# Performance work log

Measured on AMD Instinct MI355X. Metric: run time of the kernel, lower is better.

Reference implementation:

```python
import jax, jax.numpy as jnp
import numpy as np

N = 100000   # nodes
E = 1600000  # edges
G = 64       # graphs in batch
IN, H, F1, OUT = 3, 64, 256, 10
EPS = 1e-5


def setup_inputs() -> dict:
    key = jax.random.key(0)
    ks = jax.random.split(key, 16)
    d = {}
    d["x"] = jax.random.normal(ks[0], (N, IN), dtype=jnp.float32)
    d["membership"] = jnp.sort(jax.random.randint(ks[1], (N,), 0, G))
    d["edges"] = jax.random.randint(ks[2], (2, E), 0, N)
    def lin(k, fan_in, shape):
        return jax.random.uniform(k, shape, jnp.float32, -1.0, 1.0) / np.sqrt(fan_in)
    # GraphConv1: out = lin_rel(agg) + lin_root(x); lin_root has no bias in PyG
    d["W_rel1"] = lin(ks[3], IN, (IN, H)); d["b_rel1"] = jnp.zeros((H,), jnp.float32)
    d["W_root1"] = lin(ks[4], IN, (IN, H))
    d["W_rel2"] = lin(ks[5], H, (H, H)); d["b_rel2"] = jnp.zeros((H,), jnp.float32)
    d["W_root2"] = lin(ks[6], H, (H, H))
    d["g1"] = jnp.ones((H,), jnp.float32); d["b1"] = jnp.zeros((H,), jnp.float32)
    d["g2"] = jnp.ones((H,), jnp.float32); d["b2"] = jnp.zeros((H,), jnp.float32)
    d["W_fc1"] = lin(ks[7], H, (H, F1)); d["b_fc1"] = lin(ks[8], H, (F1,))
    d["g3"] = jnp.ones((F1,), jnp.float32); d["b3"] = jnp.zeros((F1,), jnp.float32)
    d["W_fc2"] = lin(ks[9], F1, (F1, OUT)); d["b_fc2"] = lin(ks[10], F1, (OUT,))
    return d


def _bn(h, g, b):
    # BatchNorm1d in training mode: biased batch variance
    m = h.mean(axis=0)
    v = h.var(axis=0)
    return (h - m) * jax.lax.rsqrt(v + EPS) * g + b


def reference(x, membership, edges, W_rel1, b_rel1, W_root1, W_rel2, b_rel2,
              W_root2, g1, b1, g2, b2, W_fc1, b_fc1, g3, b3, W_fc2, b_fc2):
    src, dst = edges[0], edges[1]

    def gconv(h, Wr, br, Wroot):
        # message = x_j (edge_weight=None); aggr='add' at target node
        agg = jax.ops.segment_sum(h[src], dst, num_segments=N)
        return agg @ Wr + br + h @ Wroot

    h = _bn(jax.nn.relu(gconv(x, W_rel1, b_rel1, W_root1)), g1, b1)
    h = _bn(jax.nn.relu(gconv(h, W_rel2, b_rel2, W_root2)), g2, b2)
    # global mean pool over graph membership
    cnt = jax.ops.segment_sum(jnp.ones((N,), h.dtype), membership, num_segments=G)
    pooled = jax.ops.segment_sum(h, membership, num_segments=G) / jnp.maximum(cnt, 1.0)[:, None]
    z = _bn(jax.nn.relu(pooled @ W_fc1 + b_fc1), g3, b3)
    return z @ W_fc2 + b_fc2
```

## Files before the change

kernel.cpp:

```cpp
#include <hip/hip_runtime.h>
#include <hip/hip_bf16.h>

#define EPSV 1e-5f
#define BKT 128
#define NB  782
#define LPK 4096

typedef __hip_bfloat16 bf16;
typedef __attribute__((ext_vector_type(8))) short short8v;
typedef __attribute__((ext_vector_type(4))) float f32x4v;

__device__ inline void atomAddG(float* p, float v) { unsafeAtomicAdd(p, v); }
__device__ inline unsigned short f2bf(float v) {
    bf16 h = __float2bfloat16(v);
    return *reinterpret_cast<unsigned short*>(&h);
}
__device__ inline float bfu(unsigned short u) {
    return __uint_as_float(((unsigned int)u) << 16);
}

__global__ __launch_bounds__(256) void bhist_kernel(
    const int* __restrict__ edges, int* __restrict__ gbcnt,
    const float* __restrict__ x, float* __restrict__ xp, int E, int N)
{
    __shared__ int lh[NB];
    const int t = threadIdx.x;
    for (int i = t; i < NB; i += 256) lh[i] = 0;
    {
        int n = blockIdx.x * 256 + t;
        if (n < N) {
            float4 v;
            v.x = x[n * 3 + 0]; v.y = x[n * 3 + 1]; v.z = x[n * 3 + 2]; v.w = 0.f;
            *(float4*)&xp[n * 4] = v;
        }
    }
    __syncthreads();
    const int base = blockIdx.x * 4096;
    #pragma unroll
    for (int i = 0; i < 16; ++i) {
        int e = base + i * 256 + t;
        if (e < E) atomicAdd(&lh[edges[E + e] >> 7], 1);
    }
    __syncthreads();
    for (int i = t; i < NB; i += 256) {
        int c = lh[i];
        if (c) atomicAdd(&gbcnt[i], c);
    }
}

__global__ __launch_bounds__(256) void bscan_kernel(
    const int* __restrict__ gbcnt, int* __restrict__ bbase,
    int* __restrict__ gcursor, int E)
{
    __shared__ int l[256];
    const int t = threadIdx.x;
    int b0 = t * 4;
    int v0 = (b0 + 0 < NB) ? gbcnt[b0 + 0] : 0;
    int v1 = (b0 + 1 < NB) ? gbcnt[b0 + 1] : 0;
    int v2 = (b0 + 2 < NB) ? gbcnt[b0 + 2] : 0;
    int v3 = (b0 + 3 < NB) ? gbcnt[b0 + 3] : 0;
    int tot = v0 + v1 + v2 + v3;
    l[t] = tot;
    __syncthreads();
    for (int o = 1; o < 256; o <<= 1) {
        int add = (t >= o) ? l[t - o] : 0;
        __syncthreads();
        l[t] += add;
        __syncthreads();
    }
    int off = l[t] - tot;
    if (b0 + 0 < NB) { bbase[b0 + 0] = off;                gcursor[b0 + 0] = off; }
    if (b0 + 1 < NB) { bbase[b0 + 1] = off + v0;           gcursor[b0 + 1] = off + v0; }
    if (b0 + 2 < NB) { bbase[b0 + 2] = off + v0 + v1;      gcursor[b0 + 2] = off + v0 + v1; }
    if (b0 + 3 < NB) { bbase[b0 + 3] = off + v0 + v1 + v2; gcursor[b0 + 3] = off + v0 + v1 + v2; }
    if (t == 0) bbase[NB] = E;
}

__global__ __launch_bounds__(256) void bfill_kernel(
    const int* __restrict__ edges, int* __restrict__ gcursor,
    int* __restrict__ pk,
    const int* __restrict__ membership, int* __restrict__ gstart, int E, int N)
{
    __shared__ int lh[NB];
    __shared__ int lbase[NB];
    const int t = threadIdx.x;
    for (int i = t; i < NB; i += 256) lh[i] = 0;
    {
        int n = blockIdx.x * 256 + t;
        if (n <= N) {
            int mp = (n == 0) ? -1 : membership[n - 1];
            int mc = (n == N) ? 64 : membership[n];
            for (int g = mp + 1; g <= mc; ++g) gstart[g] = n;
        }
    }
    __syncthreads();
    const int base = blockIdx.x * 4096;
    int dv[16];
    #pragma unroll
    for (int i = 0; i < 16; ++i) {
        int e = base + i * 256 + t;
        dv[i] = (e < E) ? edges[E + e] : -1;
        if (dv[i] >= 0) atomicAdd(&lh[dv[i] >> 7], 1);
    }
    __syncthreads();
    for (int i = t; i < NB; i += 256) {
        int c = lh[i];
        lbase[i] = c ? atomicAdd(&gcursor[i], c) : 0;
        lh[i] = 0;
    }
    __syncthreads();
    #pragma unroll
    for (int i = 0; i < 16; ++i) {
        int e = base + i * 256 + t;
        if (dv[i] >= 0) {
            int s = edges[e];
            int b = dv[i] >> 7;
            int pos = lbase[b] + atomicAdd(&lh[b], 1);
            pk[pos] = (s << 7) | (dv[i] & 127);
        }
    }
}

__global__ __launch_bounds__(256) void bsort_kernel(
    const int* __restrict__ pk, const int* __restrict__ bbase,
    const float* __restrict__ xp,
    int* __restrict__ rowstart, int* __restrict__ srcs,
    float* __restrict__ agg1, int N, int E)
{
    __shared__ int lcnt[BKT];
    __shared__ int lscan[BKT];
    __shared__ float accx[BKT * 4];
    __shared__ int lpk[LPK];
    const int t = threadIdx.x;
    const int b = blockIdx.x;
    const int e0 = bbase[b], e1 = bbase[b + 1];
    const int cnt = e1 - e0;
    if (t < BKT) lcnt[t] = 0;
    for (int i = t; i < BKT * 4; i += 256) accx[i] = 0.f;
    for (int i = t; i < cnt && i < LPK; i += 256) lpk[i] = pk[e0 + i];
    __syncthreads();
    for (int i = t; i < cnt; i += 256) {
        int v = (i < LPK) ? lpk[i] : pk[e0 + i];
        atomicAdd(&lcnt[v & 127], 1);
    }
    __syncthreads();
    if (t < BKT) lscan[t] = lcnt[t];
    __syncthreads();
    for (int o = 1; o < BKT; o <<= 1) {
        int add = (t < BKT && t >= o) ? lscan[t - o] : 0;
        __syncthreads();
        if (t < BKT) lscan[t] += add;
        __syncthreads();
    }
    const int n0 = b * BKT;
    if (t < BKT) {
        int excl = lscan[t] - lcnt[t];
        lscan[t] = excl;
        int n = n0 + t;
        if (n <= N) rowstart[n] = e0 + excl;
        lcnt[t] = 0;
    }
    __syncthreads();
    for (int i = t; i < cnt; i += 256) {
        int v = (i < LPK) ? lpk[i] : pk[e0 + i];
        int ld = v & 127;
        int s = v >> 7;
        int pos = atomicAdd(&lcnt[ld], 1);
        srcs[e0 + lscan[ld] + pos] = s;
        float4 xv = *(const float4*)&xp[s * 4];
        atomicAdd(&accx[ld * 4 + 0], xv.x);
        atomicAdd(&accx[ld * 4 + 1], xv.y);
        atomicAdd(&accx[ld * 4 + 2], xv.z);
    }
    __syncthreads();
    for (int i = t; i < BKT * 3; i += 256) {
        int nl = i / 3, c = i - nl * 3;
        int n = n0 + nl;
        if (n < N) agg1[n * 3 + c] = accx[nl * 4 + c];
    }
}

__global__ __launch_bounds__(256) void layer1_kernel(
    const float* __restrict__ x, const float* __restrict__ agg1,
    const float* __restrict__ W_rel1, const float* __restrict__ b_rel1,
    const float* __restrict__ W_root1,
    unsigned short* __restrict__ u1b, float* __restrict__ sums, float* __restrict__ sumsq,
    int N)
{
    const int t = threadIdx.x;
    const int f = t & 63, r4 = t >> 6;
    const float wr0 = W_rel1[f], wr1 = W_rel1[64 + f], wr2 = W_rel1[128 + f];
    const float wo0 = W_root1[f], wo1 = W_root1[64 + f], wo2 = W_root1[128 + f];
    const float bb = b_rel1[f];
    float ps = 0.f, pq = 0.f;
    const int base = blockIdx.x * 128;
    for (int i = r4; i < 128; i += 4) {
        int n = base + i;
        if (n >= N) break;
        float a0 = agg1[n * 3 + 0], a1 = agg1[n * 3 + 1], a2 = agg1[n * 3 + 2];
        float x0 = x[n * 3 + 0], x1 = x[n * 3 + 1], x2 = x[n * 3 + 2];
        float v = bb;
        v = fmaf(a0, wr0, v); v = fmaf(a1, wr1, v); v = fmaf(a2, wr2, v);
        v = fmaf(x0, wo0, v); v = fmaf(x1, wo1, v); v = fmaf(x2, wo2, v);
        v = fmaxf(v, 0.f);
        u1b[n * 64 + f] = f2bf(v);
        ps += v; pq += v * v;
    }
    __shared__ float lsum[4][64], lsq[4][64];
    lsum[r4][f] = ps; lsq[r4][f] = pq;
    __syncthreads();
    if (r4 == 0) {
        float s = lsum[0][f] + lsum[1][f] + lsum[2][f] + lsum[3][f];
        float q = lsq[0][f] + lsq[1][f] + lsq[2][f] + lsq[3][f];
        atomAddG(&sums[f], s);
        atomAddG(&sumsq[f], q);
    }
}

__global__ __launch_bounds__(256) void bnfold_kernel(
    const float* __restrict__ sums1, const float* __restrict__ sumsq1,
    const float* __restrict__ g1, const float* __restrict__ b1,
    const float* __restrict__ W_rel2, const float* __restrict__ W_root2,
    const float* __restrict__ b_rel2,
    unsigned short* __restrict__ wrelp, unsigned short* __restrict__ wrootp,
    float* __restrict__ crel, float* __restrict__ croot, float invn)
{
    __shared__ float lsc[64], lsh[64];
    __shared__ float r1[4][64], r2[4][64];
    const int t = threadIdx.x, f = t & 63, kg = t >> 6;
    if (t < 64) {
        float m = sums1[t] * invn;
        float v = sumsq1[t] * invn - m * m;
        float sc = g1[t] * rsqrtf(v + EPSV);
        lsc[t] = sc;
        lsh[t] = b1[t] - m * sc;
    }
    __syncthreads();
    float c1 = 0.f, c2 = 0.f;
    for (int k = kg * 16; k < kg * 16 + 16; ++k) {
        float sc = lsc[k], sh = lsh[k];
        float w1 = W_rel2[k * 64 + f], w2 = W_root2[k * 64 + f];
        wrelp[k * 64 + f] = f2bf(sc * w1);
        wrootp[k * 64 + f] = f2bf(sc * w2);
        c1 = fmaf(sh, w1, c1); c2 = fmaf(sh, w2, c2);
    }
    r1[kg][f] = c1; r2[kg][f] = c2;
    __syncthreads();
    if (kg == 0) {
        crel[f]  = r1[0][f] + r1[1][f] + r1[2][f] + r1[3][f];
        croot[f] = r2[0][f] + r2[1][f] + r2[2][f] + r2[3][f] + b_rel2[f];
    }
}

__global__ __launch_bounds__(256) void mfma_transform_kernel(
    const unsigned short* __restrict__ u1b,
    const unsigned short* __restrict__ wrelp, const unsigned short* __restrict__ wrootp,
    const float* __restrict__ crel, const float* __restrict__ croot,
    unsigned short* __restrict__ tb, unsigned short* __restrict__ pb, int NT)
{
    const int wid = (blockIdx.x * blockDim.x + threadIdx.x) >> 6;
    const int lane = threadIdx.x & 63;
    const int q = lane >> 4, r = lane & 15;

    short8v Bf[2][8];
    float cadd[8];
    #pragma unroll
    for (int kc = 0; kc < 2; ++kc) {
        #pragma unroll
        for (int ft = 0; ft < 8; ++ft) {
            const unsigned short* W = (ft < 4) ? wrelp : wrootp;
            const int f0 = (ft & 3) * 16;
            short8v bb;
            #pragma unroll
            for (int j = 0; j < 8; ++j) {
                int k = 32 * kc + 8 * q + j;
                bb[j] = (short)W[k * 64 + f0 + r];
            }
            Bf[kc][ft] = bb;
        }
    }
    #pragma unroll
    for (int ft = 0; ft < 8; ++ft)
        cadd[ft] = (ft < 4) ? crel[(ft & 3) * 16 + r] : croot[(ft & 3) * 16 + r];

    const int totalWaves = (gridDim.x * blockDim.x) >> 6;
    for (int tile = wid; tile < NT; tile += totalWaves) {
        const int n0 = tile * 16;
        short8v A0 = *(const short8v*)&u1b[(n0 + r) * 64 + 8 * q];
        short8v A1 = *(const short8v*)&u1b[(n0 + r) * 64 + 32 + 8 * q];
        #pragma unroll
        for (int ft = 0; ft < 8; ++ft) {
            f32x4v d = {0.f, 0.f, 0.f, 0.f};
            d = __builtin_amdgcn_mfma_f32_16x16x32_bf16(A0, Bf[0][ft], d, 0, 0, 0);
            d = __builtin_amdgcn_mfma_f32_16x16x32_bf16(A1, Bf[1][ft], d, 0, 0, 0);
            unsigned short* O = (ft < 4) ? tb : pb;
            const int f0 = (ft & 3) * 16;
            const float ca = cadd[ft];
            #pragma unroll
            for (int rr = 0; rr < 4; ++rr) {
                int n = n0 + 4 * q + rr;
                O[n * 64 + f0 + r] = f2bf(d[rr] + ca);
            }
        }
    }
}

__global__ __launch_bounds__(256, 8) void gatherpool_kernel(
    const unsigned short* __restrict__ tb, const unsigned short* __restrict__ pb,
    const int* __restrict__ rowstart, const int* __restrict__ srcs,
    const int* __restrict__ membership,
    float* __restrict__ pooled, float* __restrict__ sums, float* __restrict__ sumsq,
    int N, int chunk)
{
    __shared__ float red[4][64];
    const int tid = threadIdx.x;
    const int w = tid >> 6, f = tid & 63;
    const int gw = __builtin_amdgcn_readfirstlane(blockIdx.x * 4 + w);
    const int n0 = gw * chunk;
    const int n1 = min(N, n0 + chunk);
    float ps = 0.f, pq = 0.f, pacc = 0.f;
    int curg = (n0 < N) ? membership[n0] : -1;

    for (int n = n0; n < n1; ++n) {
        int s0 = rowstart[n], s1 = rowstart[n + 1];
        float acc = bfu(pb[n * 64 + f]);
        int j = s0;
        for (; j + 15 < s1; j += 16) {
            float vs[16];
            #pragma unroll
            for (int q = 0; q < 16; ++q)
                vs[q] = bfu(tb[srcs[j + q] * 64 + f]);
            float sA = ((vs[0] + vs[1]) + (vs[2] + vs[3])) + ((vs[4] + vs[5]) + (vs[6] + vs[7]));
            float sB = ((vs[8] + vs[9]) + (vs[10] + vs[11])) + ((vs[12] + vs[13]) + (vs[14] + vs[15]));
            acc += sA + sB;
        }
        for (; j + 3 < s1; j += 4) {
            float v0 = bfu(tb[srcs[j + 0] * 64 + f]);
            float v1 = bfu(tb[srcs[j + 1] * 64 + f]);
            float v2 = bfu(tb[srcs[j + 2] * 64 + f]);
            float v3 = bfu(tb[srcs[j + 3] * 64 + f]);
            acc += (v0 + v1) + (v2 + v3);
        }
        for (; j < s1; ++j) acc += bfu(tb[srcs[j] * 64 + f]);

        acc = fmaxf(acc, 0.f);
        ps += acc; pq += acc * acc;

        int g = membership[n];
        if (g != curg) {
            atomAddG(&pooled[curg * 64 + f], pacc);
            pacc = 0.f;
            curg = g;
        }
        pacc += acc;
    }
    if (curg >= 0) atomAddG(&pooled[curg * 64 + f], pacc);

    red[w][f] = ps;
    __syncthreads();
    if (w == 0) atomAddG(&sums[f], red[0][f] + red[1][f] + red[2][f] + red[3][f]);
    __syncthreads();
    red[w][f] = pq;
    __syncthreads();
    if (w == 0) atomAddG(&sumsq[f], red[0][f] + red[1][f] + red[2][f] + red[3][f]);
}

__global__ __launch_bounds__(1024) void fc12_kernel(
    const float* __restrict__ pooled, const int* __restrict__ gstart,
    const float* __restrict__ sums2, const float* __restrict__ sumsq2,
    const float* __restrict__ g2, const float* __restrict__ b2, float invn,
    const float* __restrict__ W_fc1, const float* __restrict__ b_fc1,
    const float* __restrict__ g3, const float* __restrict__ b3,
    const float* __restrict__ W_fc2, const float* __restrict__ b_fc2,
    float* __restrict__ z, float* __restrict__ out)
{
    __shared__ float pm[4096];
    __shared__ float reds[4][256], redq[4][256];
    __shared__ float lsc[256], lsh[256];
    __shared__ float sc2[64], sh2[64];
    const int t = threadIdx.x;
    if (t < 64) {
        float m = sums2[t] * invn;
        float v = sumsq2[t] * invn - m * m;
        float sc = g2[t] * rsqrtf(v + EPSV);
        sc2[t] = sc;
        sh2[t] = b2[t] - m * sc;
    }
    __syncthreads();
    for (int i = t; i < 4096; i += 1024) {
        int g = i >> 6, f = i & 63;
        float c = fmaxf((float)(gstart[g + 1] - gstart[g]), 1.0f);
        pm[i] = fmaf(pooled[i] / c, sc2[f], sh2[f]);
    }
    __syncthreads();
    const int col = t & 255, grp = t >> 8;
    float acc[16];
    const float bc = b_fc1[col];
    #pragma unroll
    for (int g = 0; g < 16; ++g) acc[g] = bc;
    for (int k = 0; k < 64; ++k) {
        float wv = W_fc1[k * 256 + col];
        #pragma unroll
        for (int g = 0; g < 16; ++g)
            acc[g] = fmaf(pm[(grp * 16 + g) * 64 + k], wv, acc[g]);
    }
    float s = 0.f, q = 0.f;
    #pragma unroll
    for (int g = 0; g < 16; ++g) {
        acc[g] = fmaxf(acc[g], 0.f);
        s += acc[g]; q += acc[g] * acc[g];
    }
    reds[grp][col] = s; redq[grp][col] = q;
    __syncthreads();
    if (grp == 0) {
        float S = reds[0][col] + reds[1][col] + reds[2][col] + reds[3][col];
        float Q = redq[0][col] + redq[1][col] + redq[2][col] + redq[3][col];
        float m = S * (1.0f / 64.0f);
        float v = Q * (1.0f / 64.0f) - m * m;
        float sc = g3[col] * rsqrtf(v + EPSV);
        lsc[col] = sc;
        lsh[col] = b3[col] - m * sc;
    }
    __syncthreads();
    float sc = lsc[col], sh = lsh[col];
    #pragma unroll
    for (int g = 0; g < 16; ++g)
        z[(grp * 16 + g) * 256 + col] = fmaf(acc[g], sc, sh);
    __syncthreads();
    if (t < 640) {
        int g = t / 10, o = t % 10;
        float a = b_fc2[o];
        for (int c = 0; c < 256; ++c)
            a = fmaf(z[g * 256 + c], W_fc2[c * 10 + o], a);
        out[g * 10 + o] = a;
    }
}

extern "C" void kernel_launch(void* const* d_in, const int* in_sizes, int n_in,
                              void* d_out, int out_size, void* d_ws, size_t ws_size,
                              hipStream_t stream) {
    const int N = 100000, E = 1600000;

    const float* x          = (const float*)d_in[0];
    const int*   membership = (const int*)d_in[1];
    const int*   edges      = (const int*)d_in[2];
    const float* W_rel1     = (const float*)d_in[3];
    const float* b_rel1     = (const float*)d_in[4];
    const float* W_root1    = (const float*)d_in[5];
    const float* W_rel2     = (const float*)d_in[6];
    const float* b_rel2     = (const float*)d_in[7];
    const float* W_root2    = (const float*)d_in[8];
    const float* g1         = (const float*)d_in[9];
    const float* b1         = (const float*)d_in[10];
    const float* g2         = (const float*)d_in[11];
    const float* b2         = (const float*)d_in[12];
    const float* W_fc1      = (const float*)d_in[13];
    const float* b_fc1      = (const float*)d_in[14];
    const float* g3         = (const float*)d_in[15];
    const float* b3         = (const float*)d_in[16];
    const float* W_fc2      = (const float*)d_in[17];
    const float* b_fc2      = (const float*)d_in[18];

    int*   wsi      = (int*)d_ws;
    float* wsf      = (float*)d_ws;
    int*   gbcnt    = wsi + 0;
    float* stats    = wsf + 784;
    float* pooled   = wsf + 1296;
    int*   bbase    = wsi + 5392;
    int*   gcursor  = wsi + 6192;
    int*   gstart   = wsi + 6976;
    int*   rowstart = wsi + 7104;
    int*   pk       = wsi + 107168;
    int*   srcs     = wsi + 1707168;
    float* agg1     = wsf + 3307168;
    unsigned short* u1b = (unsigned short*)(wsf + 3607200);
    unsigned short* tb  = (unsigned short*)(wsf + 6807200);
    unsigned short* pb  = (unsigned short*)(wsf + 10007200);
    unsigned short* wrelp  = (unsigned short*)(wsf + 13207200);
    unsigned short* wrootp = (unsigned short*)(wsf + 13209248);
    float* crel     = wsf + 13211296;
    float* croot    = wsf + 13211360;
    float* z        = wsf + 13211424;
    float* xp       = wsf + 13227808;

    float* sums1  = stats + 0;
    float* sumsq1 = stats + 64;
    float* sums2  = stats + 128;
    float* sumsq2 = stats + 192;

    hipMemsetAsync(d_ws, 0, (size_t)(784 + 512 + 4096) * 4, stream);

    const int EB = (E + 4095) / 4096;
    bhist_kernel<<<EB, 256, 0, stream>>>(edges, gbcnt, x, xp, E, N);
    bscan_kernel<<<1, 256, 0, stream>>>(gbcnt, bbase, gcursor, E);
    bfill_kernel<<<EB, 256, 0, stream>>>(edges, gcursor, pk, membership, gstart, E, N);
    bsort_kernel<<<NB, 256, 0, stream>>>(pk, bbase, xp, rowstart, srcs, agg1, N, E);

    layer1_kernel<<<(N + 127) / 128, 256, 0, stream>>>(
        x, agg1, W_rel1, b_rel1, W_root1, u1b, sums1, sumsq1, N);

    bnfold_kernel<<<1, 256, 0, stream>>>(sums1, sumsq1, g1, b1,
                                         W_rel2, W_root2, b_rel2,
                                         wrelp, wrootp, crel, croot, 1.0f / N);
    mfma_transform_kernel<<<512, 256, 0, stream>>>(
        u1b, wrelp, wrootp, crel, croot, tb, pb, N / 16);

    {
        const int GRID2 = 2048;
        int chunk = (N + GRID2 * 4 - 1) / (GRID2 * 4);
        gatherpool_kernel<<<GRID2, 256, 0, stream>>>(
            tb, pb, rowstart, srcs, membership, pooled, sums2, sumsq2, N, chunk);
    }

    fc12_kernel<<<1, 1024, 0, stream>>>(pooled, gstart, sums2, sumsq2, g2, b2, 1.0f / N,
                                        W_fc1, b_fc1, g3, b3, W_fc2, b_fc2,
                                        z, (float*)d_out);
}
```

Before: 244.1 us.

## Fuse layer1 into bucket sort, move gstart to hist, enlarge fill tiles

Layer-1 GraphConv, ReLU and the BN statistics now run inside bsort_kernel, straight from the shared-memory aggregation buffer, so the agg1 round trip and one kernel launch go away. The gstart computation moves from bfill to bhist. bfill now processes 8192 edges per block with 32 registers per thread, and the gatherpool grid doubles. The trade-offs are higher register pressure in bfill and more shared memory and work per bsort block.

```diff
diff --git a/kernel.cpp b/kernel.cpp
--- a/kernel.cpp
+++ b/kernel.cpp
@@ -21,7 +21,8 @@
 
 __global__ __launch_bounds__(256) void bhist_kernel(
     const int* __restrict__ edges, int* __restrict__ gbcnt,
-    const float* __restrict__ x, float* __restrict__ xp, int E, int N)
+    const float* __restrict__ x, float* __restrict__ xp,
+    const int* __restrict__ membership, int* __restrict__ gstart, int E, int N)
 {
     __shared__ int lh[NB];
     const int t = threadIdx.x;
@@ -33,6 +34,11 @@
             v.x = x[n * 3 + 0]; v.y = x[n * 3 + 1]; v.z = x[n * 3 + 2]; v.w = 0.f;
             *(float4*)&xp[n * 4] = v;
         }
+        if (n <= N) {
+            int mp = (n == 0) ? -1 : membership[n - 1];
+            int mc = (n == N) ? 64 : membership[n];
+            for (int g = mp + 1; g <= mc; ++g) gstart[g] = n;
+        }
     }
     __syncthreads();
     const int base = blockIdx.x * 4096;
@@ -78,26 +84,17 @@
 
 __global__ __launch_bounds__(256) void bfill_kernel(
     const int* __restrict__ edges, int* __restrict__ gcursor,
-    int* __restrict__ pk,
-    const int* __restrict__ membership, int* __restrict__ gstart, int E, int N)
+    int* __restrict__ pk, int E)
 {
     __shared__ int lh[NB];
     __shared__ int lbase[NB];
     const int t = threadIdx.x;
     for (int i = t; i < NB; i += 256) lh[i] = 0;
-    {
-        int n = blockIdx.x * 256 + t;
-        if (n <= N) {
-            int mp = (n == 0) ? -1 : membership[n - 1];
-            int mc = (n == N) ? 64 : membership[n];
-            for (int g = mp + 1; g <= mc; ++g) gstart[g] = n;
-        }
-    }
-    __syncthreads();
-    const int base = blockIdx.x * 4096;
-    int dv[16];
-    #pragma unroll
-    for (int i = 0; i < 16; ++i) {
+    __syncthreads();
+    const int base = blockIdx.x * 8192;
+    int dv[32];
+    #pragma unroll
+    for (int i = 0; i < 32; ++i) {
         int e = base + i * 256 + t;
         dv[i] = (e < E) ? edges[E + e] : -1;
         if (dv[i] >= 0) atomicAdd(&lh[dv[i] >> 7], 1);
@@ -110,7 +107,7 @@
     }
     __syncthreads();
     #pragma unroll
-    for (int i = 0; i < 16; ++i) {
+    for (int i = 0; i < 32; ++i) {
         int e = base + i * 256 + t;
         if (dv[i] >= 0) {
             int s = edges[e];
@@ -124,13 +121,17 @@
 __global__ __launch_bounds__(256) void bsort_kernel(
     const int* __restrict__ pk, const int* __restrict__ bbase,
     const float* __restrict__ xp,
+    const float* __restrict__ W_rel1, const float* __restrict__ b_rel1,
+    const float* __restrict__ W_root1,
     int* __restrict__ rowstart, int* __restrict__ srcs,
-    float* __restrict__ agg1, int N, int E)
+    unsigned short* __restrict__ u1b, float* __restrict__ sums, float* __restrict__ sumsq,
+    int N, int E)
 {
     __shared__ int lcnt[BKT];
     __shared__ int lscan[BKT];
     __shared__ float accx[BKT * 4];
     __shared__ int lpk[LPK];
+    __shared__ float red[4][64];
     const int t = threadIdx.x;
     const int b = blockIdx.x;
     const int e0 = bbase[b], e1 = bbase[b + 1];
@@ -173,48 +174,32 @@
         atomicAdd(&accx[ld * 4 + 2], xv.z);
     }
     __syncthreads();
-    for (int i = t; i < BKT * 3; i += 256) {
-        int nl = i / 3, c = i - nl * 3;
-        int n = n0 + nl;
-        if (n < N) agg1[n * 3 + c] = accx[nl * 4 + c];
-    }
-}
-
-__global__ __launch_bounds__(256) void layer1_kernel(
-    const float* __restrict__ x, const float* __restrict__ agg1,
-    const float* __restrict__ W_rel1, const float* __restrict__ b_rel1,
-    const float* __restrict__ W_root1,
-    unsigned short* __restrict__ u1b, float* __restrict__ sums, float* __restrict__ sumsq,
-    int N)
-{
-    const int t = threadIdx.x;
+
     const int f = t & 63, r4 = t >> 6;
     const float wr0 = W_rel1[f], wr1 = W_rel1[64 + f], wr2 = W_rel1[128 + f];
     const float wo0 = W_root1[f], wo1 = W_root1[64 + f], wo2 = W_root1[128 + f];
     const float bb = b_rel1[f];
     float ps = 0.f, pq = 0.f;
-    const int base = blockIdx.x * 128;
-    for (int i = r4; i < 128; i += 4) {
-        int n = base + i;
-        if (n >= N) break;
-        float a0 = agg1[n * 3 + 0], a1 = agg1[n * 3 + 1], a2 = agg1[n * 3 + 2];
-        float x0 = x[n * 3 + 0], x1 = x[n * 3 + 1], x2 = x[n * 3 + 2];
-        float v = bb;
-        v = fmaf(a0, wr0, v); v = fmaf(a1, wr1, v); v = fmaf(a2, wr2, v);
-        v = fmaf(x0, wo0, v); v = fmaf(x1, wo1, v); v = fmaf(x2, wo2, v);
-        v = fmaxf(v, 0.f);
-        u1b[n * 64 + f] = f2bf(v);
-        ps += v; pq += v * v;
-    }
-    __shared__ float lsum[4][64], lsq[4][64];
-    lsum[r4][f] = ps; lsq[r4][f] = pq;
-    __syncthreads();
-    if (r4 == 0) {
-        float s = lsum[0][f] + lsum[1][f] + lsum[2][f] + lsum[3][f];
-        float q = lsq[0][f] + lsq[1][f] + lsq[2][f] + lsq[3][f];
-        atomAddG(&sums[f], s);
-        atomAddG(&sumsq[f], q);
-    }
+    for (int i = r4; i < BKT; i += 4) {
+        int n = n0 + i;
+        if (n < N) {
+            float4 xv = *(const float4*)&xp[n * 4];
+            float a0 = accx[i * 4 + 0], a1 = accx[i * 4 + 1], a2 = accx[i * 4 + 2];
+            float v = bb;
+            v = fmaf(a0, wr0, v); v = fmaf(a1, wr1, v); v = fmaf(a2, wr2, v);
+            v = fmaf(xv.x, wo0, v); v = fmaf(xv.y, wo1, v); v = fmaf(xv.z, wo2, v);
+            v = fmaxf(v, 0.f);
+            u1b[n * 64 + f] = f2bf(v);
+            ps += v; pq += v * v;
+        }
+    }
+    red[r4][f] = ps;
+    __syncthreads();
+    if (r4 == 0) atomAddG(&sums[f], red[0][f] + red[1][f] + red[2][f] + red[3][f]);
+    __syncthreads();
+    red[r4][f] = pq;
+    __syncthreads();
+    if (r4 == 0) atomAddG(&sumsq[f], red[0][f] + red[1][f] + red[2][f] + red[3][f]);
 }
 
 __global__ __launch_bounds__(256) void bnfold_kernel(
@@ -472,7 +457,6 @@
     int*   rowstart = wsi + 7104;
     int*   pk       = wsi + 107168;
     int*   srcs     = wsi + 1707168;
-    float* agg1     = wsf + 3307168;
     unsigned short* u1b = (unsigned short*)(wsf + 3607200);
     unsigned short* tb  = (unsigned short*)(wsf + 6807200);
     unsigned short* pb  = (unsigned short*)(wsf + 10007200);
@@ -491,13 +475,12 @@
     hipMemsetAsync(d_ws, 0, (size_t)(784 + 512 + 4096) * 4, stream);
 
     const int EB = (E + 4095) / 4096;
-    bhist_kernel<<<EB, 256, 0, stream>>>(edges, gbcnt, x, xp, E, N);
+    const int EB2 = (E + 8191) / 8192;
+    bhist_kernel<<<EB, 256, 0, stream>>>(edges, gbcnt, x, xp, membership, gstart, E, N);
     bscan_kernel<<<1, 256, 0, stream>>>(gbcnt, bbase, gcursor, E);
-    bfill_kernel<<<EB, 256, 0, stream>>>(edges, gcursor, pk, membership, gstart, E, N);
-    bsort_kernel<<<NB, 256, 0, stream>>>(pk, bbase, xp, rowstart, srcs, agg1, N, E);
-
-    layer1_kernel<<<(N + 127) / 128, 256, 0, stream>>>(
-        x, agg1, W_rel1, b_rel1, W_root1, u1b, sums1, sumsq1, N);
+    bfill_kernel<<<EB2, 256, 0, stream>>>(edges, gcursor, pk, E);
+    bsort_kernel<<<NB, 256, 0, stream>>>(pk, bbase, xp, W_rel1, b_rel1, W_root1,
+                                         rowstart, srcs, u1b, sums1, sumsq1, N, E);
 
     bnfold_kernel<<<1, 256, 0, stream>>>(sums1, sumsq1, g1, b1,
                                          W_rel2, W_root2, b_rel2,
@@ -506,7 +489,7 @@
         u1b, wrelp, wrootp, crel, croot, tb, pb, N / 16);
 
     {
-        const int GRID2 = 2048;
+        const int GRID2 = 4096;
         int chunk = (N + GRID2 * 4 - 1) / (GRID2 * 4);
         gatherpool_kernel<<<GRID2, 256, 0, stream>>>(
             tb, pb, rowstart, srcs, membership, pooled, sums2, sumsq2, N, chunk);
```

After: 280.2 us. +14.8%, slower.
